# Optimization experiments

Hardware: AMD Instinct MI355X
Metric: run time of the kernel (lower is better)

## Reference

```python
import jax, jax.numpy as jnp
import numpy as np

N, E, B, D, L = 60000, 120000, 512, 256, 6
NUM_TYPES = 25
GEN_EPS = 1e-7
LN_EPS = 1e-5


def setup_inputs() -> dict:
    key = jax.random.key(0)
    ks = jax.random.split(key, 12)
    s = 0.02
    x = jax.random.randint(ks[0], (N, 1), 0, NUM_TYPES)
    edge_index = jax.random.randint(ks[1], (2, E), 0, N)
    edge_attr = jax.random.uniform(ks[2], (E,), dtype=jnp.float32)
    batch = jnp.sort(jax.random.randint(ks[3], (N,), 0, B))
    node_emb = jax.random.normal(ks[4], (NUM_TYPES, D), dtype=jnp.float32) * s
    ln_scale = jnp.ones((L, D), jnp.float32)
    ln_bias = jnp.zeros((L, D), jnp.float32)
    wl_w = jax.random.normal(ks[5], (L, 1, D), dtype=jnp.float32) * s
    wl_b = jnp.zeros((L, D), jnp.float32)
    conv_w = jax.random.normal(ks[6], (L, D, D), dtype=jnp.float32) * s
    conv_b = jnp.zeros((L, D), jnp.float32)
    dims = [L * D, L * D // 2, L * D // 4, L * D // 8, 1]  # 1536->768->384->192->1
    ro = {}
    for i in range(4):
        ro[f'ro_w{i}'] = jax.random.normal(ks[7 + i], (dims[i], dims[i + 1]), dtype=jnp.float32) * s
        ro[f'ro_b{i}'] = jnp.zeros((dims[i + 1],), jnp.float32)
    return dict(x=x, edge_index=edge_index, edge_attr=edge_attr, batch=batch,
                node_emb=node_emb, ln_scale=ln_scale, ln_bias=ln_bias,
                wl_w=wl_w, wl_b=wl_b, conv_w=conv_w, conv_b=conv_b, **ro)


def _layer_norm(h, scale, bias):
    mu = h.mean(-1, keepdims=True)
    var = ((h - mu) ** 2).mean(-1, keepdims=True)
    return (h - mu) * jax.lax.rsqrt(var + LN_EPS) * scale + bias


def _forward(edge_attr, node_emb, ln_scale, ln_bias, wl_w, wl_b, conv_w, conv_b,
             ro_w0, ro_b0, ro_w1, ro_b1, ro_w2, ro_b2, ro_w3, ro_b3,
             x, edge_index, batch):
    h = node_emb[x].sum(axis=1)                      # [N, D] node features
    src, dst = edge_index[0], edge_index[1]
    ea = edge_attr[:, None]                          # [E, 1]
    outs = []
    for i in range(L):
        y = _layer_norm(h, ln_scale[i], ln_bias[i])
        eproj = ea @ wl_w[i] + wl_b[i]               # [E, D] edge features
        msg = jax.nn.relu(y[src] + eproj) + GEN_EPS  # GENConv message
        m = jax.ops.segment_max(msg, dst, num_segments=N)     # per-dst max (softmax aggr)
        w = jnp.exp(msg - m[dst])
        denom = jax.ops.segment_sum(w, dst, num_segments=N)
        agg = jax.ops.segment_sum(msg * w, dst, num_segments=N) / jnp.maximum(denom, 1e-16)
        h = jax.nn.relu((agg + y) @ conv_w[i] + conv_b[i])     # residual + MLP(1 layer), then EncoderLayer relu
        outs.append(jax.ops.segment_sum(h, batch, num_segments=B))  # global_add_pool
    z = jnp.concatenate(outs, axis=1)                # [B, L*D]
    for w_, b_ in ((ro_w0, ro_b0), (ro_w1, ro_b1), (ro_w2, ro_b2)):
        z = jax.nn.gelu(z @ w_ + b_, approximate=False)
    return z @ ro_w3 + ro_b3                         # [B, 1]


def reference(x, edge_index, edge_attr, batch, node_emb, ln_scale, ln_bias,
              wl_w, wl_b, conv_w, conv_b,
              ro_w0, ro_b0, ro_w1, ro_b1, ro_w2, ro_b2, ro_w3, ro_b3):
    return _forward(edge_attr, node_emb, ln_scale, ln_bias, wl_w, wl_b, conv_w, conv_b,
                    ro_w0, ro_b0, ro_w1, ro_b1, ro_w2, ro_b2, ro_w3, ro_b3,
                    x, edge_index, batch)
```

## Files before the change

kernel.cpp:

```cpp
#include <hip/hip_runtime.h>
#include <hip/hip_bf16.h>
#include <math.h>

#define N_NODES 60000
#define N_EDGES 120000
#define N_BATCH 512
#define DIM 256
#define N_LAYERS 6
#define GEN_EPS 1e-7f
#define LN_EPS 1e-5f
#define NBLK ((N_NODES + 255) / 256)

typedef __attribute__((ext_vector_type(8))) short bf16x8;
typedef __attribute__((ext_vector_type(4))) float f32x4;

#define GLOBAL_AS __attribute__((address_space(1)))
#define LDS_AS __attribute__((address_space(3)))

__device__ __forceinline__ unsigned short f2bf(float f) {
    unsigned u = __float_as_uint(f);
    u = (u + 0x7fffu + ((u >> 16) & 1u)) >> 16;
    return (unsigned short)u;
}
__device__ __forceinline__ float bf2f(unsigned short u) {
    return __uint_as_float((unsigned)u << 16);
}

__global__ void embed_ln_kernel(const int* __restrict__ x, const float* __restrict__ emb,
                                const float* __restrict__ lnsc, const float* __restrict__ lnbi,
                                unsigned short* __restrict__ h, unsigned short* __restrict__ y) {
    int row = blockIdx.x * 4 + (threadIdx.x >> 6);
    int lane = threadIdx.x & 63;
    if (row >= N_NODES) return;
    int d = lane * 4;
    int type = x[row];
    float4 v = *(const float4*)(emb + (size_t)type * DIM + d);
    ushort4 ho;
    ho.x = f2bf(v.x); ho.y = f2bf(v.y); ho.z = f2bf(v.z); ho.w = f2bf(v.w);
    *(ushort4*)(h + (size_t)row * DIM + d) = ho;
    float s = v.x + v.y + v.z + v.w;
    float q = v.x * v.x + v.y * v.y + v.z * v.z + v.w * v.w;
    #pragma unroll
    for (int off = 32; off > 0; off >>= 1) {
        s += __shfl_xor(s, off, 64);
        q += __shfl_xor(q, off, 64);
    }
    float mu = s * (1.0f / DIM);
    float var = q * (1.0f / DIM) - mu * mu;
    float r = rsqrtf(fmaxf(var, 0.0f) + LN_EPS);
    float4 sc = *(const float4*)(lnsc + d);
    float4 bi = *(const float4*)(lnbi + d);
    ushort4 o;
    o.x = f2bf((v.x - mu) * r * sc.x + bi.x);
    o.y = f2bf((v.y - mu) * r * sc.y + bi.y);
    o.z = f2bf((v.z - mu) * r * sc.z + bi.z);
    o.w = f2bf((v.w - mu) * r * sc.w + bi.w);
    *(ushort4*)(y + (size_t)row * DIM + d) = o;
}

__global__ void hist_kernel(const int* __restrict__ ei, int* __restrict__ deg) {
    int e = blockIdx.x * 256 + threadIdx.x;
    if (e >= N_EDGES) return;
    atomicAdd(&deg[ei[N_EDGES + e]], 1);
}

__global__ void scan1_kernel(const int* __restrict__ deg, int* __restrict__ part) {
    __shared__ int sm[256];
    int i = blockIdx.x * 256 + threadIdx.x;
    int t = threadIdx.x;
    sm[t] = (i < N_NODES) ? deg[i] : 0;
    __syncthreads();
    for (int off = 128; off > 0; off >>= 1) {
        if (t < off) sm[t] += sm[t + off];
        __syncthreads();
    }
    if (t == 0) part[blockIdx.x] = sm[0];
}

__global__ void scan2_kernel(int* __restrict__ part) {
    __shared__ int sm[256];
    int t = threadIdx.x;
    int v = (t < NBLK) ? part[t] : 0;
    sm[t] = v;
    __syncthreads();
    for (int off = 1; off < 256; off <<= 1) {
        int add = (t >= off) ? sm[t - off] : 0;
        __syncthreads();
        sm[t] += add;
        __syncthreads();
    }
    if (t < NBLK) part[t] = sm[t] - v;
}

__global__ void scan3_kernel(const int* __restrict__ deg, const int* __restrict__ part,
                             int* __restrict__ ofs, int* __restrict__ cursor) {
    __shared__ int sm[256];
    int i = blockIdx.x * 256 + threadIdx.x;
    int t = threadIdx.x;
    int v = (i < N_NODES) ? deg[i] : 0;
    sm[t] = v;
    __syncthreads();
    for (int off = 1; off < 256; off <<= 1) {
        int add = (t >= off) ? sm[t - off] : 0;
        __syncthreads();
        sm[t] += add;
        __syncthreads();
    }
    int excl = part[blockIdx.x] + sm[t] - v;
    if (i < N_NODES) {
        ofs[i] = excl;
        cursor[i] = excl;
        if (i == N_NODES - 1) ofs[N_NODES] = excl + v;
    }
}

__global__ void scatter_kernel(const int* __restrict__ ei, const float* __restrict__ ea,
                               int* __restrict__ cursor, int* __restrict__ edge_src,
                               float* __restrict__ edge_a) {
    int e = blockIdx.x * 256 + threadIdx.x;
    if (e >= N_EDGES) return;
    int dst = ei[N_EDGES + e];
    int pos = atomicAdd(&cursor[dst], 1);
    edge_src[pos] = ei[e];
    edge_a[pos] = ea[e];
}

__global__ void bofs_kernel(const int* __restrict__ batch, int* __restrict__ bofs) {
    int b = blockIdx.x * 256 + threadIdx.x;
    if (b > N_BATCH) return;
    int lo = 0, hi = N_NODES;
    while (lo < hi) {
        int mid = (lo + hi) >> 1;
        if (batch[mid] < b) lo = mid + 1; else hi = mid;
    }
    bofs[b] = lo;
}

__global__ void agg_kernel(const int* __restrict__ ofs, const int* __restrict__ edge_src,
                           const float* __restrict__ edge_a, const unsigned short* __restrict__ y,
                           const float* __restrict__ wlw, const float* __restrict__ wlb,
                           unsigned short* __restrict__ A) {
    const float LOG2E = 1.4426950408889634f;
    int dst = blockIdx.x * 4 + (threadIdx.x >> 6);
    int lane = threadIdx.x & 63;
    if (dst >= N_NODES) return;
    int d = lane * 4;
    float4 wv = *(const float4*)(wlw + d);
    float4 bv = *(const float4*)(wlb + d);
    int lo = ofs[dst], hi = ofs[dst + 1];
    float den0 = 0.f, den1 = 0.f, den2 = 0.f, den3 = 0.f;
    float ag0 = 0.f, ag1 = 0.f, ag2 = 0.f, ag3 = 0.f;
    int e = lo;
    for (; e + 1 < hi; e += 2) {
        int s0 = edge_src[e];
        int s1 = edge_src[e + 1];
        float a0 = edge_a[e];
        float a1 = edge_a[e + 1];
        ushort4 u0 = *(const ushort4*)(y + (size_t)s0 * DIM + d);
        ushort4 u1 = *(const ushort4*)(y + (size_t)s1 * DIM + d);
        float g0 = fmaxf(bf2f(u0.x) + a0 * wv.x + bv.x, 0.0f) + GEN_EPS;
        float g1 = fmaxf(bf2f(u0.y) + a0 * wv.y + bv.y, 0.0f) + GEN_EPS;
        float g2 = fmaxf(bf2f(u0.z) + a0 * wv.z + bv.z, 0.0f) + GEN_EPS;
        float g3 = fmaxf(bf2f(u0.w) + a0 * wv.w + bv.w, 0.0f) + GEN_EPS;
        float h0 = fmaxf(bf2f(u1.x) + a1 * wv.x + bv.x, 0.0f) + GEN_EPS;
        float h1 = fmaxf(bf2f(u1.y) + a1 * wv.y + bv.y, 0.0f) + GEN_EPS;
        float h2 = fmaxf(bf2f(u1.z) + a1 * wv.z + bv.z, 0.0f) + GEN_EPS;
        float h3 = fmaxf(bf2f(u1.w) + a1 * wv.w + bv.w, 0.0f) + GEN_EPS;
        float w0 = exp2f(g0 * LOG2E), w1 = exp2f(g1 * LOG2E);
        float w2 = exp2f(g2 * LOG2E), w3 = exp2f(g3 * LOG2E);
        float x0 = exp2f(h0 * LOG2E), x1 = exp2f(h1 * LOG2E);
        float x2 = exp2f(h2 * LOG2E), x3 = exp2f(h3 * LOG2E);
        den0 += w0 + x0; ag0 += g0 * w0 + h0 * x0;
        den1 += w1 + x1; ag1 += g1 * w1 + h1 * x1;
        den2 += w2 + x2; ag2 += g2 * w2 + h2 * x2;
        den3 += w3 + x3; ag3 += g3 * w3 + h3 * x3;
    }
    if (e < hi) {
        int src = edge_src[e];
        float a = edge_a[e];
        ushort4 u = *(const ushort4*)(y + (size_t)src * DIM + d);
        float g0 = fmaxf(bf2f(u.x) + a * wv.x + bv.x, 0.0f) + GEN_EPS;
        float g1 = fmaxf(bf2f(u.y) + a * wv.y + bv.y, 0.0f) + GEN_EPS;
        float g2 = fmaxf(bf2f(u.z) + a * wv.z + bv.z, 0.0f) + GEN_EPS;
        float g3 = fmaxf(bf2f(u.w) + a * wv.w + bv.w, 0.0f) + GEN_EPS;
        float w0 = exp2f(g0 * LOG2E), w1 = exp2f(g1 * LOG2E);
        float w2 = exp2f(g2 * LOG2E), w3 = exp2f(g3 * LOG2E);
        den0 += w0; ag0 += g0 * w0;
        den1 += w1; ag1 += g1 * w1;
        den2 += w2; ag2 += g2 * w2;
        den3 += w3; ag3 += g3 * w3;
    }
    ushort4 ud = *(const ushort4*)(y + (size_t)dst * DIM + d);
    float o0 = ag0 / fmaxf(den0, 1e-16f) + bf2f(ud.x);
    float o1 = ag1 / fmaxf(den1, 1e-16f) + bf2f(ud.y);
    float o2 = ag2 / fmaxf(den2, 1e-16f) + bf2f(ud.z);
    float o3 = ag3 / fmaxf(den3, 1e-16f) + bf2f(ud.w);
    ushort4 o;
    o.x = f2bf(o0); o.y = f2bf(o1); o.z = f2bf(o2); o.w = f2bf(o3);
    *(ushort4*)(A + (size_t)dst * DIM + d) = o;
}

__global__ void wt_kernel(const float* __restrict__ w, unsigned short* __restrict__ wt) {
    int idx = blockIdx.x * 256 + threadIdx.x;
    if (idx >= N_LAYERS * DIM * DIM) return;
    int l = idx >> 16;
    int rem = idx & 0xFFFF;
    int n = rem >> 8;
    int k = rem & 0xFF;
    wt[idx] = f2bf(w[(size_t)l * DIM * DIM + (size_t)k * DIM + n]);
}

__global__ __launch_bounds__(256) void wt_ro_t_kernel(const float* __restrict__ w,
                                                      unsigned short* __restrict__ wth,
                                                      unsigned short* __restrict__ wtl,
                                                      int K, int N) {
    __shared__ float tile[32][33];
    int k0 = blockIdx.x * 32, n0 = blockIdx.y * 32;
    int tx = threadIdx.x & 31, ty = threadIdx.x >> 5;
    #pragma unroll
    for (int i = 0; i < 4; i++)
        tile[ty + 8 * i][tx] = w[(size_t)(k0 + ty + 8 * i) * N + n0 + tx];
    __syncthreads();
    #pragma unroll
    for (int i = 0; i < 4; i++) {
        int n = ty + 8 * i;
        float v = tile[tx][n];
        unsigned short hh = f2bf(v);
        size_t idx = (size_t)(n0 + n) * K + k0 + tx;
        wth[idx] = hh;
        wtl[idx] = f2bf(v - bf2f(hh));
    }
}

__global__ __launch_bounds__(256) void mfma_gemm_kernel(const unsigned short* __restrict__ A,
                                                        const unsigned short* __restrict__ WT,
                                                        const float* __restrict__ bias,
                                                        const float* __restrict__ lnsc,
                                                        const float* __restrict__ lnbi,
                                                        unsigned short* __restrict__ Ch,
                                                        unsigned short* __restrict__ Cy,
                                                        int do_ln, int M) {
    __shared__ alignas(16) unsigned short Asmem[64 * 256];
    __shared__ float lsum[64][4];
    __shared__ float lsq[64][4];
    int lane = threadIdx.x & 63;
    int w = threadIdx.x >> 6;
    int m_base = blockIdx.x * 64;
    int n_base = w * 64;
    int frow = lane & 15;
    int kp = (lane >> 4) * 8;

    #pragma unroll
    for (int it = 0; it < 8; it++) {
        int C = (it * 4 + w) * 64 + lane;
        int row = C >> 5;
        int b0 = (C & 31) * 16;
        int kb = b0 ^ ((row & 7) << 4);
        int grow = m_base + row;
        if (grow >= M) grow = M - 1;
        const unsigned short* gsrc = A + (size_t)grow * DIM + (kb >> 1);
        unsigned short* ldst = Asmem + (size_t)(it * 4 + w) * 512;
        __builtin_amdgcn_global_load_lds((const GLOBAL_AS void*)gsrc,
                                         (LDS_AS void*)ldst, 16, 0, 0);
    }

    bf16x8 breg[8][4];
    #pragma unroll
    for (int s = 0; s < 8; s++)
        #pragma unroll
        for (int j = 0; j < 4; j++)
            breg[s][j] = *(const bf16x8*)(WT + (size_t)(n_base + j * 16 + frow) * DIM
                                          + s * 32 + kp);

    __syncthreads();

    f32x4 acc[4][4];
    #pragma unroll
    for (int j = 0; j < 4; j++)
        #pragma unroll
        for (int i = 0; i < 4; i++) acc[j][i] = (f32x4){0.f, 0.f, 0.f, 0.f};

    #pragma unroll
    for (int s = 0; s < 8; s++) {
        bf16x8 a[4];
        #pragma unroll
        for (int i = 0; i < 4; i++) {
            int r = i * 16 + frow;
            int bb = (s * 64 + (lane >> 4) * 16) ^ ((r & 7) << 4);
            a[i] = *(const bf16x8*)((const char*)Asmem + r * 512 + bb);
        }
        #pragma unroll
        for (int j = 0; j < 4; j++)
            #pragma unroll
            for (int i = 0; i < 4; i++)
                acc[j][i] = __builtin_amdgcn_mfma_f32_16x16x32_bf16(breg[s][j], a[i],
                                                                    acc[j][i], 0, 0, 0);
    }

    int mcol = lane & 15;
    int ng = (lane >> 4) * 4;

    float psum[4], psq[4];
    #pragma unroll
    for (int i = 0; i < 4; i++) { psum[i] = 0.f; psq[i] = 0.f; }

    #pragma unroll
    for (int i = 0; i < 4; i++) {
        int gm = m_base + i * 16 + mcol;
        #pragma unroll
        for (int j = 0; j < 4; j++) {
            int n0 = n_base + j * 16 + ng;
            float4 bb = *(const float4*)(bias + n0);
            float v0 = fmaxf(acc[j][i][0] + bb.x, 0.0f);
            float v1 = fmaxf(acc[j][i][1] + bb.y, 0.0f);
            float v2 = fmaxf(acc[j][i][2] + bb.z, 0.0f);
            float v3 = fmaxf(acc[j][i][3] + bb.w, 0.0f);
            acc[j][i][0] = v0; acc[j][i][1] = v1; acc[j][i][2] = v2; acc[j][i][3] = v3;
            psum[i] += v0 + v1 + v2 + v3;
            psq[i] += v0 * v0 + v1 * v1 + v2 * v2 + v3 * v3;
            if (gm < M) {
                ushort4 o;
                o.x = f2bf(v0); o.y = f2bf(v1); o.z = f2bf(v2); o.w = f2bf(v3);
                *(ushort4*)(Ch + (size_t)gm * DIM + n0) = o;
            }
        }
    }

    if (do_ln) {
        #pragma unroll
        for (int i = 0; i < 4; i++) {
            float s = psum[i], q = psq[i];
            s += __shfl_xor(s, 16, 64); q += __shfl_xor(q, 16, 64);
            s += __shfl_xor(s, 32, 64); q += __shfl_xor(q, 32, 64);
            if ((lane >> 4) == 0) {
                lsum[i * 16 + mcol][w] = s;
                lsq[i * 16 + mcol][w] = q;
            }
        }
        __syncthreads();
        #pragma unroll
        for (int i = 0; i < 4; i++) {
            int lr = i * 16 + mcol;
            float s = lsum[lr][0] + lsum[lr][1] + lsum[lr][2] + lsum[lr][3];
            float q = lsq[lr][0] + lsq[lr][1] + lsq[lr][2] + lsq[lr][3];
            float mu = s * (1.0f / DIM);
            float var = q * (1.0f / DIM) - mu * mu;
            float rs = rsqrtf(fmaxf(var, 0.0f) + LN_EPS);
            int gm = m_base + i * 16 + mcol;
            if (gm < M) {
                #pragma unroll
                for (int j = 0; j < 4; j++) {
                    int n0 = n_base + j * 16 + ng;
                    float4 sc = *(const float4*)(lnsc + n0);
                    float4 bi = *(const float4*)(lnbi + n0);
                    ushort4 o;
                    o.x = f2bf((acc[j][i][0] - mu) * rs * sc.x + bi.x);
                    o.y = f2bf((acc[j][i][1] - mu) * rs * sc.y + bi.y);
                    o.z = f2bf((acc[j][i][2] - mu) * rs * sc.z + bi.z);
                    o.w = f2bf((acc[j][i][3] - mu) * rs * sc.w + bi.w);
                    *(ushort4*)(Cy + (size_t)gm * DIM + n0) = o;
                }
            }
        }
    }
}

__global__ __launch_bounds__(256) void mfma_ro_kernel(const unsigned short* __restrict__ Ah,
                                                      const unsigned short* __restrict__ Al,
                                                      const unsigned short* __restrict__ WTh,
                                                      const unsigned short* __restrict__ WTl,
                                                      const float* __restrict__ bias,
                                                      unsigned short* __restrict__ Ch,
                                                      unsigned short* __restrict__ Cl,
                                                      int K, int Nc) {
    __shared__ float red[4][256];
    int lane = threadIdx.x & 63;
    int wave = threadIdx.x >> 6;
    int m0 = blockIdx.x * 16;
    int n0 = blockIdx.y * 16;
    int frow = lane & 15;
    int kp = (lane >> 4) * 8;
    int kc = K >> 2;
    int kbase = wave * kc;

    f32x4 acc = (f32x4){0.f, 0.f, 0.f, 0.f};
    const unsigned short* aph = Ah + (size_t)(m0 + frow) * K + kbase + kp;
    const unsigned short* apl = Al + (size_t)(m0 + frow) * K + kbase + kp;
    const unsigned short* bph = WTh + (size_t)(n0 + frow) * K + kbase + kp;
    const unsigned short* bpl = WTl + (size_t)(n0 + frow) * K + kbase + kp;
    #pragma unroll 4
    for (int k0 = 0; k0 < kc; k0 += 32) {
        bf16x8 ah = *(const bf16x8*)(aph + k0);
        bf16x8 al = *(const bf16x8*)(apl + k0);
        bf16x8 bh = *(const bf16x8*)(bph + k0);
        bf16x8 bl = *(const bf16x8*)(bpl + k0);
        acc = __builtin_amdgcn_mfma_f32_16x16x32_bf16(ah, bh, acc, 0, 0, 0);
        acc = __builtin_amdgcn_mfma_f32_16x16x32_bf16(ah, bl, acc, 0, 0, 0);
        acc = __builtin_amdgcn_mfma_f32_16x16x32_bf16(al, bh, acc, 0, 0, 0);
    }

    *(f32x4*)&red[wave][lane * 4] = acc;
    __syncthreads();
    if (wave == 0) {
        f32x4 a0 = *(const f32x4*)&red[0][lane * 4];
        f32x4 a1 = *(const f32x4*)&red[1][lane * 4];
        f32x4 a2 = *(const f32x4*)&red[2][lane * 4];
        f32x4 a3 = *(const f32x4*)&red[3][lane * 4];
        int ccol = lane & 15;
        int crow = (lane >> 4) * 4;
        float bb = bias[n0 + ccol];
        #pragma unroll
        for (int r = 0; r < 4; r++) {
            float v = a0[r] + a1[r] + a2[r] + a3[r] + bb;
            v = 0.5f * v * (1.0f + erff(v * 0.70710678118f));
            unsigned short hh = f2bf(v);
            size_t idx = (size_t)(m0 + crow + r) * Nc + n0 + ccol;
            Ch[idx] = hh;
            Cl[idx] = f2bf(v - bf2f(hh));
        }
    }
}

__global__ __launch_bounds__(256) void pool_kernel(const unsigned short* __restrict__ h,
                                                   const int* __restrict__ bofs,
                                                   unsigned short* __restrict__ outs_h,
                                                   unsigned short* __restrict__ outs_l,
                                                   int layer) {
    __shared__ float red[16][68];
    int b = blockIdx.x;
    int cb = blockIdx.y;
    int way = threadIdx.x >> 4;
    int li = threadIdx.x & 15;
    int col = cb * 64 + li * 4;
    int lo = bofs[b], hi = bofs[b + 1];
    float4 s = make_float4(0.f, 0.f, 0.f, 0.f);
    for (int n = lo + way; n < hi; n += 16) {
        ushort4 u = *(const ushort4*)(h + (size_t)n * DIM + col);
        s.x += bf2f(u.x); s.y += bf2f(u.y); s.z += bf2f(u.z); s.w += bf2f(u.w);
    }
    *(float4*)(&red[way][li * 4]) = s;
    __syncthreads();
    if (threadIdx.x < 64) {
        int t = threadIdx.x;
        float val = 0.f;
        #pragma unroll
        for (int k = 0; k < 16; k++) val += red[k][t];
        size_t idx = (size_t)b * (N_LAYERS * DIM) + layer * DIM + cb * 64 + t;
        unsigned short hh = f2bf(val);
        outs_h[idx] = hh;
        outs_l[idx] = f2bf(val - bf2f(hh));
    }
}

__global__ void final_kernel(const unsigned short* __restrict__ zh,
                             const unsigned short* __restrict__ zl,
                             const float* __restrict__ w,
                             const float* __restrict__ b, float* __restrict__ out) {
    int m = blockIdx.x * 64 + threadIdx.x;
    if (m >= N_BATCH) return;
    float s = 0.f;
    for (int k = 0; k < 192; k++)
        s += (bf2f(zh[(size_t)m * 192 + k]) + bf2f(zl[(size_t)m * 192 + k])) * w[k];
    out[m] = s + b[0];
}

__global__ void ws_sentinel_kernel(float* __restrict__ out) {
    int t = blockIdx.x * 256 + threadIdx.x;
    if (t < N_BATCH) out[t] = 1.0e6f;
}

extern "C" void kernel_launch(void* const* d_in, const int* in_sizes, int n_in,
                              void* d_out, int out_size, void* d_ws, size_t ws_size,
                              hipStream_t stream) {
    const int*   x        = (const int*)d_in[0];
    const int*   ei       = (const int*)d_in[1];
    const float* ea       = (const float*)d_in[2];
    const int*   batch    = (const int*)d_in[3];
    const float* node_emb = (const float*)d_in[4];
    const float* ln_scale = (const float*)d_in[5];
    const float* ln_bias  = (const float*)d_in[6];
    const float* wl_w     = (const float*)d_in[7];
    const float* wl_b     = (const float*)d_in[8];
    const float* conv_w   = (const float*)d_in[9];
    const float* conv_b   = (const float*)d_in[10];
    const float* ro_w0    = (const float*)d_in[11];
    const float* ro_b0    = (const float*)d_in[12];
    const float* ro_w1    = (const float*)d_in[13];
    const float* ro_b1    = (const float*)d_in[14];
    const float* ro_w2    = (const float*)d_in[15];
    const float* ro_b2    = (const float*)d_in[16];
    const float* ro_w3    = (const float*)d_in[17];
    const float* ro_b3    = (const float*)d_in[18];
    float* out = (float*)d_out;

    const size_t ND = (size_t)N_NODES * DIM;
    char* p = (char*)d_ws;
    unsigned short* hy_buf = (unsigned short*)p;  p += ND * sizeof(unsigned short);
    unsigned short* y_buf = (unsigned short*)p;   p += ND * sizeof(unsigned short);
    unsigned short* A_buf = (unsigned short*)p;   p += ND * sizeof(unsigned short);
    unsigned short* outs_h = (unsigned short*)p;  p += (size_t)N_BATCH * 1536 * sizeof(unsigned short);
    unsigned short* outs_l = (unsigned short*)p;  p += (size_t)N_BATCH * 1536 * sizeof(unsigned short);
    unsigned short* z1h = (unsigned short*)p;     p += (size_t)N_BATCH * 768 * sizeof(unsigned short);
    unsigned short* z1l = (unsigned short*)p;     p += (size_t)N_BATCH * 768 * sizeof(unsigned short);
    unsigned short* z2h = (unsigned short*)p;     p += (size_t)N_BATCH * 384 * sizeof(unsigned short);
    unsigned short* z2l = (unsigned short*)p;     p += (size_t)N_BATCH * 384 * sizeof(unsigned short);
    unsigned short* z3h = (unsigned short*)p;     p += (size_t)N_BATCH * 192 * sizeof(unsigned short);
    unsigned short* z3l = (unsigned short*)p;     p += (size_t)N_BATCH * 192 * sizeof(unsigned short);
    unsigned short* wt_buf = (unsigned short*)p;  p += (size_t)N_LAYERS * DIM * DIM * sizeof(unsigned short);
    unsigned short* wt0h = (unsigned short*)p;    p += (size_t)768 * 1536 * sizeof(unsigned short);
    unsigned short* wt0l = (unsigned short*)p;    p += (size_t)768 * 1536 * sizeof(unsigned short);
    unsigned short* wt1h = (unsigned short*)p;    p += (size_t)384 * 768 * sizeof(unsigned short);
    unsigned short* wt1l = (unsigned short*)p;    p += (size_t)384 * 768 * sizeof(unsigned short);
    unsigned short* wt2h = (unsigned short*)p;    p += (size_t)192 * 384 * sizeof(unsigned short);
    unsigned short* wt2l = (unsigned short*)p;    p += (size_t)192 * 384 * sizeof(unsigned short);
    float* edge_a = (float*)p;                    p += (size_t)N_EDGES * sizeof(float);
    int* deg = (int*)p;                           p += (size_t)N_NODES * sizeof(int);
    int* part = (int*)p;                          p += (size_t)NBLK * sizeof(int);
    int* ofs = (int*)p;                           p += (size_t)(N_NODES + 1) * sizeof(int);
    int* cursor = (int*)p;                        p += (size_t)N_NODES * sizeof(int);
    int* edge_src = (int*)p;                      p += (size_t)N_EDGES * sizeof(int);
    int* bofs = (int*)p;                          p += (size_t)(N_BATCH + 1) * sizeof(int);
    size_t need = (size_t)(p - (char*)d_ws);
    if (ws_size < need) {
        ws_sentinel_kernel<<<2, 256, 0, stream>>>(out);
        return;
    }

    int eb = (N_EDGES + 255) / 256;

    hipMemsetAsync(deg, 0, N_NODES * sizeof(int), stream);
    hist_kernel<<<eb, 256, 0, stream>>>(ei, deg);
    scan1_kernel<<<NBLK, 256, 0, stream>>>(deg, part);
    scan2_kernel<<<1, 256, 0, stream>>>(part);
    scan3_kernel<<<NBLK, 256, 0, stream>>>(deg, part, ofs, cursor);
    scatter_kernel<<<eb, 256, 0, stream>>>(ei, ea, cursor, edge_src, edge_a);
    bofs_kernel<<<3, 256, 0, stream>>>(batch, bofs);
    wt_kernel<<<(N_LAYERS * DIM * DIM + 255) / 256, 256, 0, stream>>>(conv_w, wt_buf);
    wt_ro_t_kernel<<<dim3(1536 / 32, 768 / 32), 256, 0, stream>>>(ro_w0, wt0h, wt0l, 1536, 768);
    wt_ro_t_kernel<<<dim3(768 / 32, 384 / 32), 256, 0, stream>>>(ro_w1, wt1h, wt1l, 768, 384);
    wt_ro_t_kernel<<<dim3(384 / 32, 192 / 32), 256, 0, stream>>>(ro_w2, wt2h, wt2l, 384, 192);

    int row_blocks = (N_NODES + 3) / 4;
    int gemm_blocks = (N_NODES + 63) / 64;

    embed_ln_kernel<<<row_blocks, 256, 0, stream>>>(x, node_emb, ln_scale, ln_bias, hy_buf, y_buf);

    for (int i = 0; i < N_LAYERS; i++) {
        agg_kernel<<<row_blocks, 256, 0, stream>>>(ofs, edge_src, edge_a, y_buf,
                                                   wl_w + i * DIM, wl_b + i * DIM, A_buf);
        int nl = (i + 1 < N_LAYERS) ? (i + 1) : i;
        mfma_gemm_kernel<<<gemm_blocks, 256, 0, stream>>>(A_buf, wt_buf + (size_t)i * DIM * DIM,
                                                          conv_b + i * DIM,
                                                          ln_scale + nl * DIM, ln_bias + nl * DIM,
                                                          hy_buf, y_buf,
                                                          (i + 1 < N_LAYERS) ? 1 : 0, N_NODES);
        pool_kernel<<<dim3(N_BATCH, 4), 256, 0, stream>>>(hy_buf, bofs, outs_h, outs_l, i);
    }

    mfma_ro_kernel<<<dim3(32, 48), 256, 0, stream>>>(outs_h, outs_l, wt0h, wt0l, ro_b0,
                                                     z1h, z1l, 1536, 768);
    mfma_ro_kernel<<<dim3(32, 24), 256, 0, stream>>>(z1h, z1l, wt1h, wt1l, ro_b1,
                                                     z2h, z2l, 768, 384);
    mfma_ro_kernel<<<dim3(32, 12), 256, 0, stream>>>(z2h, z2l, wt2h, wt2l, ro_b2,
                                                     z3h, z3l, 384, 192);
    final_kernel<<<(N_BATCH + 63) / 64, 64, 0, stream>>>(z3h, z3l, ro_w3, ro_b3, out);
}
```

Baseline: 553.2 us.

## Fuse global add pooling into GEMM epilogue with atomics, drop h buffer

The per-layer pooling kernel and the bf16 store of h are removed. The GEMM epilogue now reduces its output rows per batch segment using wave shuffles and atomically adds the sums into an fp32 pooled buffer. A final kernel splits that buffer into bf16 hi/lo parts. Separately, the GEMM's register-prefetched B fragments are replaced with per-k-step loads inside the MFMA loop, which cuts register pressure but exposes load latency. This avoids writing and re-reading a 60000x256 buffer every layer, at the cost of fp32 atomics and nondeterministic summation order.

```diff
diff --git a/kernel.cpp b/kernel.cpp
--- a/kernel.cpp
+++ b/kernel.cpp
@@ -28,16 +28,13 @@
 
 __global__ void embed_ln_kernel(const int* __restrict__ x, const float* __restrict__ emb,
                                 const float* __restrict__ lnsc, const float* __restrict__ lnbi,
-                                unsigned short* __restrict__ h, unsigned short* __restrict__ y) {
+                                unsigned short* __restrict__ y) {
     int row = blockIdx.x * 4 + (threadIdx.x >> 6);
     int lane = threadIdx.x & 63;
     if (row >= N_NODES) return;
     int d = lane * 4;
     int type = x[row];
     float4 v = *(const float4*)(emb + (size_t)type * DIM + d);
-    ushort4 ho;
-    ho.x = f2bf(v.x); ho.y = f2bf(v.y); ho.z = f2bf(v.z); ho.w = f2bf(v.w);
-    *(ushort4*)(h + (size_t)row * DIM + d) = ho;
     float s = v.x + v.y + v.z + v.w;
     float q = v.x * v.x + v.y * v.y + v.z * v.z + v.w * v.w;
     #pragma unroll
@@ -123,17 +120,6 @@
     int pos = atomicAdd(&cursor[dst], 1);
     edge_src[pos] = ei[e];
     edge_a[pos] = ea[e];
-}
-
-__global__ void bofs_kernel(const int* __restrict__ batch, int* __restrict__ bofs) {
-    int b = blockIdx.x * 256 + threadIdx.x;
-    if (b > N_BATCH) return;
-    int lo = 0, hi = N_NODES;
-    while (lo < hi) {
-        int mid = (lo + hi) >> 1;
-        if (batch[mid] < b) lo = mid + 1; else hi = mid;
-    }
-    bofs[b] = lo;
 }
 
 __global__ void agg_kernel(const int* __restrict__ ofs, const int* __restrict__ edge_src,
@@ -237,12 +223,15 @@
                                                         const float* __restrict__ bias,
                                                         const float* __restrict__ lnsc,
                                                         const float* __restrict__ lnbi,
-                                                        unsigned short* __restrict__ Ch,
+                                                        const int* __restrict__ batch,
+                                                        float* __restrict__ outs_f32,
+                                                        int layer,
                                                         unsigned short* __restrict__ Cy,
                                                         int do_ln, int M) {
     __shared__ alignas(16) unsigned short Asmem[64 * 256];
     __shared__ float lsum[64][4];
     __shared__ float lsq[64][4];
+    __shared__ int batch_lds[64];
     int lane = threadIdx.x & 63;
     int w = threadIdx.x >> 6;
     int m_base = blockIdx.x * 64;
@@ -263,14 +252,10 @@
         __builtin_amdgcn_global_load_lds((const GLOBAL_AS void*)gsrc,
                                          (LDS_AS void*)ldst, 16, 0, 0);
     }
-
-    bf16x8 breg[8][4];
-    #pragma unroll
-    for (int s = 0; s < 8; s++)
-        #pragma unroll
-        for (int j = 0; j < 4; j++)
-            breg[s][j] = *(const bf16x8*)(WT + (size_t)(n_base + j * 16 + frow) * DIM
-                                          + s * 32 + kp);
+    if (threadIdx.x < 64) {
+        int gm = m_base + threadIdx.x;
+        batch_lds[threadIdx.x] = batch[gm < M ? gm : (M - 1)];
+    }
 
     __syncthreads();
 
@@ -282,7 +267,7 @@
 
     #pragma unroll
     for (int s = 0; s < 8; s++) {
-        bf16x8 a[4];
+        bf16x8 a[4], b[4];
         #pragma unroll
         for (int i = 0; i < 4; i++) {
             int r = i * 16 + frow;
@@ -291,9 +276,12 @@
         }
         #pragma unroll
         for (int j = 0; j < 4; j++)
+            b[j] = *(const bf16x8*)(WT + (size_t)(n_base + j * 16 + frow) * DIM + s * 32 + kp);
+        #pragma unroll
+        for (int j = 0; j < 4; j++)
             #pragma unroll
             for (int i = 0; i < 4; i++)
-                acc[j][i] = __builtin_amdgcn_mfma_f32_16x16x32_bf16(breg[s][j], a[i],
+                acc[j][i] = __builtin_amdgcn_mfma_f32_16x16x32_bf16(b[j], a[i],
                                                                     acc[j][i], 0, 0, 0);
     }
 
@@ -306,7 +294,6 @@
 
     #pragma unroll
     for (int i = 0; i < 4; i++) {
-        int gm = m_base + i * 16 + mcol;
         #pragma unroll
         for (int j = 0; j < 4; j++) {
             int n0 = n_base + j * 16 + ng;
@@ -318,10 +305,64 @@
             acc[j][i][0] = v0; acc[j][i][1] = v1; acc[j][i][2] = v2; acc[j][i][3] = v3;
             psum[i] += v0 + v1 + v2 + v3;
             psq[i] += v0 * v0 + v1 * v1 + v2 * v2 + v3 * v3;
-            if (gm < M) {
-                ushort4 o;
-                o.x = f2bf(v0); o.y = f2bf(v1); o.z = f2bf(v2); o.w = f2bf(v3);
-                *(ushort4*)(Ch + (size_t)gm * DIM + n0) = o;
+        }
+    }
+
+    float* outbase = outs_f32 + (size_t)layer * DIM;
+    if (batch_lds[0] == batch_lds[63]) {
+        int seg = batch_lds[0];
+        #pragma unroll
+        for (int j = 0; j < 4; j++) {
+            float t0 = 0.f, t1 = 0.f, t2 = 0.f, t3 = 0.f;
+            #pragma unroll
+            for (int i = 0; i < 4; i++) {
+                int gm = m_base + i * 16 + mcol;
+                if (gm < M) {
+                    t0 += acc[j][i][0]; t1 += acc[j][i][1];
+                    t2 += acc[j][i][2]; t3 += acc[j][i][3];
+                }
+            }
+            #pragma unroll
+            for (int off = 1; off < 16; off <<= 1) {
+                t0 += __shfl_xor(t0, off, 64);
+                t1 += __shfl_xor(t1, off, 64);
+                t2 += __shfl_xor(t2, off, 64);
+                t3 += __shfl_xor(t3, off, 64);
+            }
+            if (mcol == 0) {
+                float* op = outbase + (size_t)seg * (N_LAYERS * DIM) + n_base + j * 16 + ng;
+                atomicAdd(op + 0, t0); atomicAdd(op + 1, t1);
+                atomicAdd(op + 2, t2); atomicAdd(op + 3, t3);
+            }
+        }
+    } else {
+        #pragma unroll
+        for (int i = 0; i < 4; i++) {
+            int segA = batch_lds[i * 16];
+            int segB = batch_lds[i * 16 + 15];
+            int myseg = batch_lds[i * 16 + mcol];
+            int gm = m_base + i * 16 + mcol;
+            for (int seg = segA; seg <= segB; seg++) {
+                bool mine = (myseg == seg) && (gm < M);
+                #pragma unroll
+                for (int j = 0; j < 4; j++) {
+                    float t0 = mine ? acc[j][i][0] : 0.f;
+                    float t1 = mine ? acc[j][i][1] : 0.f;
+                    float t2 = mine ? acc[j][i][2] : 0.f;
+                    float t3 = mine ? acc[j][i][3] : 0.f;
+                    #pragma unroll
+                    for (int off = 1; off < 16; off <<= 1) {
+                        t0 += __shfl_xor(t0, off, 64);
+                        t1 += __shfl_xor(t1, off, 64);
+                        t2 += __shfl_xor(t2, off, 64);
+                        t3 += __shfl_xor(t3, off, 64);
+                    }
+                    if (mcol == 0) {
+                        float* op = outbase + (size_t)seg * (N_LAYERS * DIM) + n_base + j * 16 + ng;
+                        atomicAdd(op + 0, t0); atomicAdd(op + 1, t1);
+                        atomicAdd(op + 2, t2); atomicAdd(op + 3, t3);
+                    }
+                }
             }
         }
     }
@@ -365,6 +406,17 @@
     }
 }
 
+__global__ void conv_outs_kernel(const float* __restrict__ outs_f32,
+                                 unsigned short* __restrict__ oh,
+                                 unsigned short* __restrict__ ol) {
+    int idx = blockIdx.x * 256 + threadIdx.x;
+    if (idx >= N_BATCH * N_LAYERS * DIM) return;
+    float v = outs_f32[idx];
+    unsigned short hh = f2bf(v);
+    oh[idx] = hh;
+    ol[idx] = f2bf(v - bf2f(hh));
+}
+
 __global__ __launch_bounds__(256) void mfma_ro_kernel(const unsigned short* __restrict__ Ah,
                                                       const unsigned short* __restrict__ Al,
                                                       const unsigned short* __restrict__ WTh,
@@ -418,37 +470,6 @@
             Ch[idx] = hh;
             Cl[idx] = f2bf(v - bf2f(hh));
         }
-    }
-}
-
-__global__ __launch_bounds__(256) void pool_kernel(const unsigned short* __restrict__ h,
-                                                   const int* __restrict__ bofs,
-                                                   unsigned short* __restrict__ outs_h,
-                                                   unsigned short* __restrict__ outs_l,
-                                                   int layer) {
-    __shared__ float red[16][68];
-    int b = blockIdx.x;
-    int cb = blockIdx.y;
-    int way = threadIdx.x >> 4;
-    int li = threadIdx.x & 15;
-    int col = cb * 64 + li * 4;
-    int lo = bofs[b], hi = bofs[b + 1];
-    float4 s = make_float4(0.f, 0.f, 0.f, 0.f);
-    for (int n = lo + way; n < hi; n += 16) {
-        ushort4 u = *(const ushort4*)(h + (size_t)n * DIM + col);
-        s.x += bf2f(u.x); s.y += bf2f(u.y); s.z += bf2f(u.z); s.w += bf2f(u.w);
-    }
-    *(float4*)(&red[way][li * 4]) = s;
-    __syncthreads();
-    if (threadIdx.x < 64) {
-        int t = threadIdx.x;
-        float val = 0.f;
-        #pragma unroll
-        for (int k = 0; k < 16; k++) val += red[k][t];
-        size_t idx = (size_t)b * (N_LAYERS * DIM) + layer * DIM + cb * 64 + t;
-        unsigned short hh = f2bf(val);
-        outs_h[idx] = hh;
-        outs_l[idx] = f2bf(val - bf2f(hh));
     }
 }
 
@@ -495,9 +516,9 @@
 
     const size_t ND = (size_t)N_NODES * DIM;
     char* p = (char*)d_ws;
-    unsigned short* hy_buf = (unsigned short*)p;  p += ND * sizeof(unsigned short);
     unsigned short* y_buf = (unsigned short*)p;   p += ND * sizeof(unsigned short);
     unsigned short* A_buf = (unsigned short*)p;   p += ND * sizeof(unsigned short);
+    float* outs_f32 = (float*)p;                  p += (size_t)N_BATCH * 1536 * sizeof(float);
     unsigned short* outs_h = (unsigned short*)p;  p += (size_t)N_BATCH * 1536 * sizeof(unsigned short);
     unsigned short* outs_l = (unsigned short*)p;  p += (size_t)N_BATCH * 1536 * sizeof(unsigned short);
     unsigned short* z1h = (unsigned short*)p;     p += (size_t)N_BATCH * 768 * sizeof(unsigned short);
@@ -519,7 +540,6 @@
     int* ofs = (int*)p;                           p += (size_t)(N_NODES + 1) * sizeof(int);
     int* cursor = (int*)p;                        p += (size_t)N_NODES * sizeof(int);
     int* edge_src = (int*)p;                      p += (size_t)N_EDGES * sizeof(int);
-    int* bofs = (int*)p;                          p += (size_t)(N_BATCH + 1) * sizeof(int);
     size_t need = (size_t)(p - (char*)d_ws);
     if (ws_size < need) {
         ws_sentinel_kernel<<<2, 256, 0, stream>>>(out);
@@ -529,12 +549,12 @@
     int eb = (N_EDGES + 255) / 256;
 
     hipMemsetAsync(deg, 0, N_NODES * sizeof(int), stream);
+    hipMemsetAsync(outs_f32, 0, (size_t)N_BATCH * 1536 * sizeof(float), stream);
     hist_kernel<<<eb, 256, 0, stream>>>(ei, deg);
     scan1_kernel<<<NBLK, 256, 0, stream>>>(deg, part);
     scan2_kernel<<<1, 256, 0, stream>>>(part);
     scan3_kernel<<<NBLK, 256, 0, stream>>>(deg, part, ofs, cursor);
     scatter_kernel<<<eb, 256, 0, stream>>>(ei, ea, cursor, edge_src, edge_a);
-    bofs_kernel<<<3, 256, 0, stream>>>(batch, bofs);
     wt_kernel<<<(N_LAYERS * DIM * DIM + 255) / 256, 256, 0, stream>>>(conv_w, wt_buf);
     wt_ro_t_kernel<<<dim3(1536 / 32, 768 / 32), 256, 0, stream>>>(ro_w0, wt0h, wt0l, 1536, 768);
     wt_ro_t_kernel<<<dim3(768 / 32, 384 / 32), 256, 0, stream>>>(ro_w1, wt1h, wt1l, 768, 384);
@@ -543,7 +563,7 @@
     int row_blocks = (N_NODES + 3) / 4;
     int gemm_blocks = (N_NODES + 63) / 64;
 
-    embed_ln_kernel<<<row_blocks, 256, 0, stream>>>(x, node_emb, ln_scale, ln_bias, hy_buf, y_buf);
+    embed_ln_kernel<<<row_blocks, 256, 0, stream>>>(x, node_emb, ln_scale, ln_bias, y_buf);
 
     for (int i = 0; i < N_LAYERS; i++) {
         agg_kernel<<<row_blocks, 256, 0, stream>>>(ofs, edge_src, edge_a, y_buf,
@@ -552,10 +572,11 @@
         mfma_gemm_kernel<<<gemm_blocks, 256, 0, stream>>>(A_buf, wt_buf + (size_t)i * DIM * DIM,
                                                           conv_b + i * DIM,
                                                           ln_scale + nl * DIM, ln_bias + nl * DIM,
-                                                          hy_buf, y_buf,
+                                                          batch, outs_f32, i, y_buf,
                                                           (i + 1 < N_LAYERS) ? 1 : 0, N_NODES);
-        pool_kernel<<<dim3(N_BATCH, 4), 256, 0, stream>>>(hy_buf, bofs, outs_h, outs_l, i);
-    }
+    }
+
+    conv_outs_kernel<<<(N_BATCH * 1536 + 255) / 256, 256, 0, stream>>>(outs_f32, outs_h, outs_l);
 
     mfma_ro_kernel<<<dim3(32, 48), 256, 0, stream>>>(outs_h, outs_l, wt0h, wt0l, ro_b0,
                                                      z1h, z1l, 1536, 768);
```

New measurement: 547.7 us. About the same (-1.0%).
